# Kernel optimization log

Hardware: AMD Instinct MI355X
Metric: run time of the kernel (lower is better)

Reference implementation:

```python
import jax, jax.numpy as jnp
import numpy as np

N = 50000   # nodes
E = 640000  # edges
IN = 256    # in_dim
H = 128     # hidden
OUT = 40    # out_dim
EPS = 1e-5  # BatchNorm eps


def setup_inputs() -> dict:
    key = jax.random.key(0)
    ks = jax.random.split(key, 14)
    x = jax.random.normal(ks[0], (N, IN), jnp.float32)
    edge_index = jax.random.randint(ks[1], (2, E), 0, N)
    def lin(k, fan_in, shape):
        return jax.random.normal(k, shape, jnp.float32) / np.float32(np.sqrt(fan_in))
    return {
        "x": x,
        "edge_index": edge_index,
        # block 0 (256 -> 128, has res_proj)
        "W0": lin(ks[2], IN, (IN, H)),
        "b0": jnp.zeros((H,), jnp.float32),
        "g0": jnp.ones((H,), jnp.float32),
        "be0": jnp.zeros((H,), jnp.float32),
        "pW": lin(ks[3], IN, (IN, H)),
        "pb": jnp.zeros((H,), jnp.float32),
        # block 1 (128 -> 128, identity residual)
        "W1": lin(ks[4], H, (H, H)),
        "b1": jnp.zeros((H,), jnp.float32),
        "g1": jnp.ones((H,), jnp.float32),
        "be1": jnp.zeros((H,), jnp.float32),
        # head
        "hW": lin(ks[5], H, (H, OUT)),
        "hb": jnp.zeros((OUT,), jnp.float32),
    }


def _gcn_conv(x, W, b, edge_index):
    """GCNConv(improved=True): x' = D^-1/2 (A + 2I) D^-1/2 (x W) + b."""
    h = x @ W  # [N, dout]
    row, col = edge_index[0], edge_index[1]  # source -> target
    # degree of A + 2I (edge_weight = 1, self-loop fill = 2.0)
    deg = jnp.zeros((N,), h.dtype).at[col].add(1.0) + 2.0
    dis = jax.lax.rsqrt(deg)  # deg > 0 always (self-loops)
    norm = dis[row] * dis[col]  # [E]
    # neighbor aggregation: scatter-add normalized messages to targets
    agg = jnp.zeros_like(h).at[col].add(norm[:, None] * h[row])
    # self-loop contribution with weight 2.0
    agg = agg + (2.0 * dis * dis)[:, None] * h
    return agg + b


def _bn(x, gamma, beta):
    # batch statistics (training-mode BatchNorm math), biased variance
    m = jnp.mean(x, axis=0)
    v = jnp.mean(jnp.square(x - m), axis=0)
    return (x - m) * jax.lax.rsqrt(v + EPS) * gamma + beta


def reference(x, edge_index, W0, b0, g0, be0, pW, pb, W1, b1, g1, be1, hW, hb):
    # block 0: conv -> bn -> relu -> (+ res_proj(x))
    out = jax.nn.relu(_bn(_gcn_conv(x, W0, b0, edge_index), g0, be0))
    x1 = out + (x @ pW + pb)
    # block 1: conv -> bn -> relu -> (+ identity)
    out = jax.nn.relu(_bn(_gcn_conv(x1, W1, b1, edge_index), g1, be1))
    x2 = out + x1
    return x2 @ hW + hb  # [N, OUT]
```

## Files before the change

kernel.cpp:

```cpp
#include <hip/hip_runtime.h>

#define H 128
#define IN_DIM 256
#define OUT_DIM 40
#define EPS 1e-5f

typedef unsigned short ushortT;
typedef __attribute__((ext_vector_type(8))) short bf16x8;
typedef __attribute__((ext_vector_type(4))) float f32x4;

static __device__ __forceinline__ ushortT f2bf(float f) {
    union { float f; unsigned u; } v; v.f = f;
    unsigned r = v.u + 0x7FFF + ((v.u >> 16) & 1);
    return (ushortT)(r >> 16);
}
static __device__ __forceinline__ unsigned pk2(float a, float b) {
    return (unsigned)f2bf(a) | ((unsigned)f2bf(b) << 16);
}
static __device__ __forceinline__ float bflo(unsigned v) {
    union { unsigned u; float f; } t; t.u = v << 16; return t.f;
}
static __device__ __forceinline__ float bfhi(unsigned v) {
    union { unsigned u; float f; } t; t.u = v & 0xFFFF0000u; return t.f;
}
static __device__ __forceinline__ float i2f(int v) {
    union { int i; float f; } t; t.i = v; return t.f;
}
static __device__ __forceinline__ int f2i(float v) {
    union { float f; int i; } t; t.f = v; return t.i;
}


__global__ __launch_bounds__(256) void count_xcd(const int* __restrict__ ei, int E, int nper,
                                                 int* __restrict__ cnt) {
    int xcd = blockIdx.x & 7;
    int nchunk = gridDim.x >> 3;
    int chunk = blockIdx.x >> 3;
    int csz = (E + nchunk - 1) / nchunk;
    int beg = chunk * csz;
    int end = min(E, beg + csz);
    for (int e = beg + (int)threadIdx.x; e < end; e += 256) {
        int c = ei[E + e];
        if (c / nper == xcd) atomicAdd(&cnt[c], 1);
    }
}

__global__ __launch_bounds__(256) void scan_block_sum(const int* __restrict__ cnt, int* __restrict__ bsum,
                                                      float* __restrict__ dis, int N) {
    __shared__ int s[256];
    int i = blockIdx.x * 256 + threadIdx.x;
    int c = (i < N) ? cnt[i] : -1;
    int v = (i < N) ? c + 1 : 0;
    if (i < N) dis[i] = rsqrtf((float)c + 2.0f);
    s[threadIdx.x] = v;
    __syncthreads();
    for (int o = 128; o > 0; o >>= 1) {
        if (threadIdx.x < o) s[threadIdx.x] += s[threadIdx.x + o];
        __syncthreads();
    }
    if (threadIdx.x == 0) bsum[blockIdx.x] = s[0];
}

__global__ void scan_tops(const int* __restrict__ bsum, int* __restrict__ boff, int* __restrict__ rowptrN, int nb) {
    __shared__ int s[256];
    int t = threadIdx.x;
    int v = (t < nb) ? bsum[t] : 0;
    s[t] = v;
    __syncthreads();
    for (int o = 1; o < 256; o <<= 1) {
        int u = (t >= o) ? s[t - o] : 0;
        __syncthreads();
        s[t] += u;
        __syncthreads();
    }
    if (t < nb) boff[t] = s[t] - v;
    if (t == 255) *rowptrN = s[255];
}

__global__ __launch_bounds__(256) void scan_final(const int* __restrict__ cnt, const int* __restrict__ boff,
                                                  const float* __restrict__ dis,
                                                  int* __restrict__ rowptr, int* __restrict__ cursor,
                                                  int2* __restrict__ recs, int N) {
    __shared__ int s[256];
    int t = threadIdx.x;
    int i = blockIdx.x * 256 + t;
    int v = (i < N) ? cnt[i] + 1 : 0;
    s[t] = v;
    __syncthreads();
    for (int o = 1; o < 256; o <<= 1) {
        int u = (t >= o) ? s[t - o] : 0;
        __syncthreads();
        s[t] += u;
        __syncthreads();
    }
    if (i < N) {
        int e = boff[blockIdx.x] + s[t] - v;
        rowptr[i] = e;
        cursor[i] = e + 1;
        float d = dis[i];
        int2 r; r.x = i; r.y = f2i(2.0f * d * d);
        recs[e] = r;
    }
}

__global__ __launch_bounds__(256) void fill_xcd(const int* __restrict__ ei, int E, int nper,
                                                const float* __restrict__ dis,
                                                int* __restrict__ cursor, int2* __restrict__ recs) {
    int xcd = blockIdx.x & 7;
    int nchunk = gridDim.x >> 3;
    int chunk = blockIdx.x >> 3;
    int csz = (E + nchunk - 1) / nchunk;
    int beg = chunk * csz;
    int end = min(E, beg + csz);
    for (int e = beg + (int)threadIdx.x; e < end; e += 256) {
        int c = ei[E + e];
        if (c / nper == xcd) {
            int r = ei[e];
            int slot = atomicAdd(&cursor[c], 1);
            int2 rec; rec.x = r; rec.y = f2i(dis[r] * dis[c]);
            recs[slot] = rec;
        }
    }
}


__global__ __launch_bounds__(256) void prep_weights(const float* __restrict__ W0, const float* __restrict__ pW,
                                                    const float* __restrict__ W1, const float* __restrict__ hW,
                                                    ushortT* __restrict__ Wt0, ushortT* __restrict__ WtP,
                                                    ushortT* __restrict__ Wt1, ushortT* __restrict__ WtH,
                                                    int* __restrict__ cnt, float* __restrict__ stats, int N) {
    int i = blockIdx.x * 256 + threadIdx.x;
    if (i < 32768) { int n = i >> 8, k = i & 255; Wt0[i] = f2bf(W0[k * 128 + n]); WtP[i] = f2bf(pW[k * 128 + n]); }
    if (i < 16384) { int n = i >> 7, k = i & 127; Wt1[i] = f2bf(W1[k * 128 + n]); }
    if (i < 6144)  { int n = i >> 7, k = i & 127; WtH[i] = (n < OUT_DIM) ? f2bf(hW[k * OUT_DIM + n]) : (ushortT)0; }
    if (i < N) cnt[i] = 0;
    if (i < 512) stats[i] = 0.f;
}


static __device__ __forceinline__ void g0_loads(const float* __restrict__ X, int brow, int kc,
                                                int tid, int N, float4 pf[4]) {
#pragma unroll
    for (int i = 0; i < 4; ++i) {
        int idx = i * 512 + tid;
        int row = idx >> 5, c4 = idx & 31;
        int gr = brow + row;
        pf[i] = make_float4(0.f, 0.f, 0.f, 0.f);
        if (gr < N) pf[i] = *(const float4*)&X[(size_t)gr * IN_DIM + kc * 128 + c4 * 4];
    }
}
static __device__ __forceinline__ void g0_write(ushortT* __restrict__ Sbuf, int tid, const float4 pf[4]) {
#pragma unroll
    for (int i = 0; i < 4; ++i) {
        int idx = i * 512 + tid;
        int row = idx >> 5, c4 = idx & 31;
        uint2 p;
        p.x = pk2(pf[i].x, pf[i].y);
        p.y = pk2(pf[i].z, pf[i].w);
        *(uint2*)&Sbuf[row * 136 + c4 * 4] = p;
    }
}

__global__ __launch_bounds__(512) void mgemm0d(const float* __restrict__ X,
                                               const ushortT* __restrict__ Wt0,
                                               const ushortT* __restrict__ WtP,
                                               const float* __restrict__ pb,
                                               ushortT* __restrict__ Oh,
                                               ushortT* __restrict__ Op,
                                               int N) {
    __shared__ __align__(16) ushortT S2[2][64 * 136];
    int tid = threadIdx.x;
    int brow = blockIdx.x * 64;
    int w = tid >> 6, lane = tid & 63;
    int lm = lane & 15, lk = lane >> 4;
    int mat = w >> 2;
    int colbase = (w & 3) * 32;
    const ushortT* Wt = mat ? WtP : Wt0;

    bf16x8 breg[2][8];
#pragma unroll
    for (int nt = 0; nt < 2; ++nt)
#pragma unroll
        for (int kk = 0; kk < 8; ++kk)
            breg[nt][kk] = *(const bf16x8*)&Wt[(size_t)(colbase + nt * 16 + lm) * IN_DIM + kk * 32 + lk * 8];
    float bb[2];
    bb[0] = mat ? pb[colbase + lm] : 0.f;
    bb[1] = mat ? pb[colbase + 16 + lm] : 0.f;

    float4 pf[4];
    g0_loads(X, brow, 0, tid, N, pf);
    g0_write(S2[0], tid, pf);
    __syncthreads();
    g0_loads(X, brow, 1, tid, N, pf);

    f32x4 acc[4][2];
#pragma unroll
    for (int mt = 0; mt < 4; ++mt)
#pragma unroll
        for (int nt = 0; nt < 2; ++nt) acc[mt][nt] = (f32x4)0.f;

#pragma unroll
    for (int kk = 0; kk < 4; ++kk) {
        bf16x8 af[4];
#pragma unroll
        for (int mt = 0; mt < 4; ++mt)
            af[mt] = *(const bf16x8*)&S2[0][(mt * 16 + lm) * 136 + kk * 32 + lk * 8];
#pragma unroll
        for (int nt = 0; nt < 2; ++nt)
#pragma unroll
            for (int mt = 0; mt < 4; ++mt)
                acc[mt][nt] = __builtin_amdgcn_mfma_f32_16x16x32_bf16(af[mt], breg[nt][kk], acc[mt][nt], 0, 0, 0);
    }
    g0_write(S2[1], tid, pf);
    __syncthreads();
#pragma unroll
    for (int kk = 0; kk < 4; ++kk) {
        bf16x8 af[4];
#pragma unroll
        for (int mt = 0; mt < 4; ++mt)
            af[mt] = *(const bf16x8*)&S2[1][(mt * 16 + lm) * 136 + kk * 32 + lk * 8];
#pragma unroll
        for (int nt = 0; nt < 2; ++nt)
#pragma unroll
            for (int mt = 0; mt < 4; ++mt)
                acc[mt][nt] = __builtin_amdgcn_mfma_f32_16x16x32_bf16(af[mt], breg[nt][4 + kk], acc[mt][nt], 0, 0, 0);
    }
    __syncthreads();
#pragma unroll
    for (int mt = 0; mt < 4; ++mt)
#pragma unroll
        for (int nt = 0; nt < 2; ++nt) {
            int col = colbase + nt * 16 + lm;
#pragma unroll
            for (int j = 0; j < 4; ++j) {
                int row = mt * 16 + lk * 4 + j;
                S2[mat][row * 136 + col] = f2bf(acc[mt][nt][j] + bb[nt]);
            }
        }
    __syncthreads();
#pragma unroll
    for (int i = 0; i < 4; ++i) {
        int idx = i * 512 + tid;
        int m2 = idx >> 10;
        int rem = idx & 1023;
        int row = rem >> 4, colq = rem & 15;
        int gr = brow + row;
        if (gr < N) {
            uint4 v = *(const uint4*)&S2[m2][row * 136 + colq * 8];
            ushortT* O = m2 ? Op : Oh;
            *(uint4*)&O[(size_t)gr * 128 + colq * 8] = v;
        }
    }
}


__global__ __launch_bounds__(512) void mgemm1_fused(const uint4* __restrict__ aggb,
                                                    const uint4* __restrict__ projb,
                                                    const float* __restrict__ stats,
                                                    const float* __restrict__ g,
                                                    const float* __restrict__ be,
                                                    const ushortT* __restrict__ Wt1,
                                                    ushortT* __restrict__ O,
                                                    uint4* __restrict__ x1b,
                                                    int N) {
    __shared__ __align__(16) ushortT S[17408];
    __shared__ float sc[128], sh[128];
    int tid = threadIdx.x;
    int brow = blockIdx.x * 128;

    if (tid < 128) {
        float mean = stats[tid] / (float)N;
        float var = stats[128 + tid] / (float)N - mean * mean;
        float inv = rsqrtf(var + EPS);
        float s = g[tid] * inv;
        sc[tid] = s;
        sh[tid] = be[tid] - mean * s;
    }
    __syncthreads();

#pragma unroll
    for (int i = 0; i < 4; ++i) {
        int idx = i * 512 + tid;
        int row = idx >> 4, q = idx & 15;
        int gr = brow + row;
        uint4 a = make_uint4(0u, 0u, 0u, 0u), p = a;
        if (gr < N) {
            size_t gidx = (size_t)gr * 16 + q;
            a = aggb[gidx];
            p = projb[gidx];
        }
        int ch = q * 8;
        float v0 = fmaxf(fmaf(bflo(a.x), sc[ch + 0], sh[ch + 0]), 0.f) + bflo(p.x);
        float v1 = fmaxf(fmaf(bfhi(a.x), sc[ch + 1], sh[ch + 1]), 0.f) + bfhi(p.x);
        float v2 = fmaxf(fmaf(bflo(a.y), sc[ch + 2], sh[ch + 2]), 0.f) + bflo(p.y);
        float v3 = fmaxf(fmaf(bfhi(a.y), sc[ch + 3], sh[ch + 3]), 0.f) + bfhi(p.y);
        float v4 = fmaxf(fmaf(bflo(a.z), sc[ch + 4], sh[ch + 4]), 0.f) + bflo(p.z);
        float v5 = fmaxf(fmaf(bfhi(a.z), sc[ch + 5], sh[ch + 5]), 0.f) + bfhi(p.z);
        float v6 = fmaxf(fmaf(bflo(a.w), sc[ch + 6], sh[ch + 6]), 0.f) + bflo(p.w);
        float v7 = fmaxf(fmaf(bfhi(a.w), sc[ch + 7], sh[ch + 7]), 0.f) + bfhi(p.w);
        uint4 pv;
        pv.x = pk2(v0, v1);
        pv.y = pk2(v2, v3);
        pv.z = pk2(v4, v5);
        pv.w = pk2(v6, v7);
        *(uint4*)&S[row * 136 + q * 8] = pv;
        if (gr < N) x1b[(size_t)gr * 16 + q] = pv;
    }
    __syncthreads();

    int w = tid >> 6, lane = tid & 63;
    int lm = lane & 15, lk = lane >> 4;
    int rh = (w >> 2) * 64;
    int colbase = (w & 3) * 32;

    bf16x8 breg[2][4];
#pragma unroll
    for (int nt = 0; nt < 2; ++nt)
#pragma unroll
        for (int ks = 0; ks < 4; ++ks)
            breg[nt][ks] = *(const bf16x8*)&Wt1[(size_t)(colbase + nt * 16 + lm) * H + ks * 32 + lk * 8];

    f32x4 acc[4][2];
#pragma unroll
    for (int mt = 0; mt < 4; ++mt)
#pragma unroll
        for (int nt = 0; nt < 2; ++nt) acc[mt][nt] = (f32x4)0.f;

#pragma unroll
    for (int ks = 0; ks < 4; ++ks) {
        bf16x8 af[4];
#pragma unroll
        for (int mt = 0; mt < 4; ++mt)
            af[mt] = *(const bf16x8*)&S[(rh + mt * 16 + lm) * 136 + ks * 32 + lk * 8];
#pragma unroll
        for (int nt = 0; nt < 2; ++nt)
#pragma unroll
            for (int mt = 0; mt < 4; ++mt)
                acc[mt][nt] = __builtin_amdgcn_mfma_f32_16x16x32_bf16(af[mt], breg[nt][ks], acc[mt][nt], 0, 0, 0);
    }

    __syncthreads();
#pragma unroll
    for (int mt = 0; mt < 4; ++mt)
#pragma unroll
        for (int nt = 0; nt < 2; ++nt) {
            int col = colbase + nt * 16 + lm;
#pragma unroll
            for (int j = 0; j < 4; ++j) {
                int row = rh + mt * 16 + lk * 4 + j;
                S[row * 136 + col] = f2bf(acc[mt][nt][j]);
            }
        }
    __syncthreads();
#pragma unroll
    for (int i = 0; i < 4; ++i) {
        int idx = i * 512 + tid;
        int row = idx >> 4, colq = idx & 15;
        int gr = brow + row;
        if (gr < N) {
            uint4 v = *(const uint4*)&S[row * 136 + colq * 8];
            *(uint4*)&O[(size_t)gr * 128 + colq * 8] = v;
        }
    }
}


__global__ __launch_bounds__(256) void aggregate_rec(const ushortT* __restrict__ h,
                                                     const int* __restrict__ rowptr,
                                                     const int2* __restrict__ recs,
                                                     ushortT* __restrict__ aggb, int N) {
    int n = blockIdx.x * 4 + (threadIdx.x >> 6);
    if (n >= N) return;
    int lane = threadIdx.x & 63;
    int half = lane >> 5, cl = lane & 31;
    int beg = rowptr[n], end = rowptr[n + 1];
    const uint2* h2 = (const uint2*)h;
    float a0 = 0.f, a1 = 0.f, a2 = 0.f, a3 = 0.f;
    float b0 = 0.f, b1 = 0.f, b2 = 0.f, b3 = 0.f;
    int idx = beg + half;
    for (; idx + 2 < end; idx += 4) {
        int2 r0 = recs[idx];
        int2 r1 = recs[idx + 2];
        uint2 v0 = h2[(size_t)r0.x * 32 + cl];
        uint2 v1 = h2[(size_t)r1.x * 32 + cl];
        float n0 = i2f(r0.y), n1 = i2f(r1.y);
        a0 = fmaf(n0, bflo(v0.x), a0); a1 = fmaf(n0, bfhi(v0.x), a1);
        a2 = fmaf(n0, bflo(v0.y), a2); a3 = fmaf(n0, bfhi(v0.y), a3);
        b0 = fmaf(n1, bflo(v1.x), b0); b1 = fmaf(n1, bfhi(v1.x), b1);
        b2 = fmaf(n1, bflo(v1.y), b2); b3 = fmaf(n1, bfhi(v1.y), b3);
    }
    if (idx < end) {
        int2 r0 = recs[idx];
        uint2 v0 = h2[(size_t)r0.x * 32 + cl];
        float n0 = i2f(r0.y);
        a0 = fmaf(n0, bflo(v0.x), a0); a1 = fmaf(n0, bfhi(v0.x), a1);
        a2 = fmaf(n0, bflo(v0.y), a2); a3 = fmaf(n0, bfhi(v0.y), a3);
    }
    a0 += b0; a1 += b1; a2 += b2; a3 += b3;
    a0 += __shfl_xor(a0, 32);
    a1 += __shfl_xor(a1, 32);
    a2 += __shfl_xor(a2, 32);
    a3 += __shfl_xor(a3, 32);
    if (half == 0) {
        uint2 o;
        o.x = pk2(a0, a1);
        o.y = pk2(a2, a3);
        ((uint2*)aggb)[(size_t)n * 32 + cl] = o;
    }
}


__global__ __launch_bounds__(256) void stats_bf(const unsigned* __restrict__ v, int totalU,
                                                float* __restrict__ sums) {
    int tid = blockIdx.x * 256 + threadIdx.x;
    int stride = gridDim.x * 256;
    float sx = 0.f, sy = 0.f, qx = 0.f, qy = 0.f;
    for (int i = tid; i < totalU; i += stride) {
        unsigned u = v[i];
        float a = bflo(u), b = bfhi(u);
        sx += a; sy += b;
        qx = fmaf(a, a, qx); qy = fmaf(b, b, qy);
    }
    __shared__ float l0[256], l1[256], l2[256], l3[256];
    int t = threadIdx.x;
    l0[t] = sx; l1[t] = sy; l2[t] = qx; l3[t] = qy;
    __syncthreads();
    if (t < 64) {
        sx = (l0[t] + l0[t + 64]) + (l0[t + 128] + l0[t + 192]);
        sy = (l1[t] + l1[t + 64]) + (l1[t + 128] + l1[t + 192]);
        qx = (l2[t] + l2[t + 64]) + (l2[t + 128] + l2[t + 192]);
        qy = (l3[t] + l3[t + 64]) + (l3[t + 128] + l3[t + 192]);
        atomicAdd(&sums[2 * t], sx);
        atomicAdd(&sums[2 * t + 1], sy);
        atomicAdd(&sums[128 + 2 * t], qx);
        atomicAdd(&sums[128 + 2 * t + 1], qy);
    }
}


__global__ __launch_bounds__(256) void head_fused(const uint4* __restrict__ aggb,
                                                  const uint4* __restrict__ x1b,
                                                  const float* __restrict__ stats,
                                                  const float* __restrict__ g,
                                                  const float* __restrict__ be,
                                                  const ushortT* __restrict__ WtH,
                                                  const float* __restrict__ hb,
                                                  float* __restrict__ out, int N) {
    __shared__ __align__(16) ushortT As[64][136];
    __shared__ __align__(16) ushortT Bs[48][136];
    __shared__ float sc[128], sh[128];

    int tid = threadIdx.x;
    int brow = blockIdx.x * 64;
    int w = tid >> 6, lane = tid & 63;
    int lm = lane & 15, lk = lane >> 4;

    if (tid < 128) {
        float mean = stats[tid] / (float)N;
        float var = stats[128 + tid] / (float)N - mean * mean;
        float inv = rsqrtf(var + EPS);
        float s = g[tid] * inv;
        sc[tid] = s;
        sh[tid] = be[tid] - mean * s;
    }
    if (tid < 192) {
        int row = tid >> 2, q = tid & 3;
        const uint4* src = (const uint4*)&WtH[(size_t)row * H + q * 32];
        uint4 a = src[0], b = src[1], c = src[2], d = src[3];
        uint4* dst = (uint4*)&Bs[row][q * 32];
        dst[0] = a; dst[1] = b; dst[2] = c; dst[3] = d;
    }
    __syncthreads();
#pragma unroll
    for (int k = 0; k < 4; ++k) {
        int idx = k * 256 + tid;
        int row = idx >> 4, colq = idx & 15;
        int gr = brow + row;
        uint4 a = make_uint4(0u, 0u, 0u, 0u), x = a;
        if (gr < N) {
            size_t gidx = (size_t)brow * 16 + idx;
            a = aggb[gidx];
            x = x1b[gidx];
        }
        int ch = colq * 8;
        float v0 = fmaxf(fmaf(bflo(a.x), sc[ch + 0], sh[ch + 0]), 0.f) + bflo(x.x);
        float v1 = fmaxf(fmaf(bfhi(a.x), sc[ch + 1], sh[ch + 1]), 0.f) + bfhi(x.x);
        float v2 = fmaxf(fmaf(bflo(a.y), sc[ch + 2], sh[ch + 2]), 0.f) + bflo(x.y);
        float v3 = fmaxf(fmaf(bfhi(a.y), sc[ch + 3], sh[ch + 3]), 0.f) + bfhi(x.y);
        float v4 = fmaxf(fmaf(bflo(a.z), sc[ch + 4], sh[ch + 4]), 0.f) + bflo(x.z);
        float v5 = fmaxf(fmaf(bfhi(a.z), sc[ch + 5], sh[ch + 5]), 0.f) + bfhi(x.z);
        float v6 = fmaxf(fmaf(bflo(a.w), sc[ch + 6], sh[ch + 6]), 0.f) + bflo(x.w);
        float v7 = fmaxf(fmaf(bfhi(a.w), sc[ch + 7], sh[ch + 7]), 0.f) + bfhi(x.w);
        uint4 pv;
        pv.x = pk2(v0, v1);
        pv.y = pk2(v2, v3);
        pv.z = pk2(v4, v5);
        pv.w = pk2(v6, v7);
        *(uint4*)&As[row][colq * 8] = pv;
    }
    __syncthreads();

    f32x4 acc[3];
#pragma unroll
    for (int nt = 0; nt < 3; ++nt) acc[nt] = (f32x4)0.f;
#pragma unroll
    for (int ks = 0; ks < 4; ++ks) {
        bf16x8 a = *(const bf16x8*)&As[w * 16 + lm][ks * 32 + lk * 8];
#pragma unroll
        for (int nt = 0; nt < 3; ++nt) {
            bf16x8 b = *(const bf16x8*)&Bs[nt * 16 + lm][ks * 32 + lk * 8];
            acc[nt] = __builtin_amdgcn_mfma_f32_16x16x32_bf16(a, b, acc[nt], 0, 0, 0);
        }
    }
#pragma unroll
    for (int nt = 0; nt < 3; ++nt) {
        int col = nt * 16 + lm;
        if (col < OUT_DIM) {
            float bbv = hb[col];
#pragma unroll
            for (int j = 0; j < 4; ++j) {
                int r = brow + w * 16 + lk * 4 + j;
                if (r < N) out[(size_t)r * OUT_DIM + col] = acc[nt][j] + bbv;
            }
        }
    }
}


extern "C" void kernel_launch(void* const* d_in, const int* in_sizes, int n_in,
                              void* d_out, int out_size, void* d_ws, size_t ws_size,
                              hipStream_t stream) {
    const float* x   = (const float*)d_in[0];
    const int*   ei  = (const int*)d_in[1];
    const float* W0  = (const float*)d_in[2];
    const float* g0  = (const float*)d_in[4];
    const float* be0 = (const float*)d_in[5];
    const float* pW  = (const float*)d_in[6];
    const float* pb  = (const float*)d_in[7];
    const float* W1  = (const float*)d_in[8];
    const float* g1  = (const float*)d_in[10];
    const float* be1 = (const float*)d_in[11];
    const float* hW  = (const float*)d_in[12];
    const float* hb  = (const float*)d_in[13];
    float* out = (float*)d_out;

    int N = in_sizes[0] / IN_DIM;
    int E = in_sizes[1] / 2;
    size_t NH = (size_t)N * H;

    ushortT* hb16   = (ushortT*)d_ws;
    ushortT* aggb   = hb16 + NH;
    ushortT* projb  = aggb + NH;
    ushortT* x1b    = projb + NH;
    float*   dis    = (float*)(x1b + NH);
    int*     cnt    = (int*)(dis + N);
    int*     rowptr = cnt + N;
    int*     cursor = rowptr + (N + 1);
    int2*    recs   = (int2*)(cursor + N);
    float*   stats  = (float*)(recs + (E + N));
    ushortT* Wt0    = (ushortT*)(stats + 512);
    ushortT* WtP    = Wt0 + 128 * 256;
    ushortT* Wt1    = WtP + 128 * 256;
    ushortT* WtH    = Wt1 + 128 * 128;
    int*     bsum   = (int*)(WtH + 48 * 128);
    int*     boff   = bsum + 256;
    float*   stats0 = stats;
    float*   stats1 = stats + 256;

    int nb = (N + 255) / 256;
    int g64 = (N + 63) / 64;
    int g128 = (N + 127) / 128;
    int gAgg = (N + 3) / 4;

    prep_weights<<<196, 256, 0, stream>>>(W0, pW, W1, hW, Wt0, WtP, Wt1, WtH, cnt, stats, N);
    count_xcd<<<2048, 256, 0, stream>>>(ei, E, (N + 7) / 8, cnt);
    scan_block_sum<<<nb, 256, 0, stream>>>(cnt, bsum, dis, N);
    scan_tops<<<1, 256, 0, stream>>>(bsum, boff, &rowptr[N], nb);
    scan_final<<<nb, 256, 0, stream>>>(cnt, boff, dis, rowptr, cursor, recs, N);
    fill_xcd<<<2048, 256, 0, stream>>>(ei, E, (N + 7) / 8, dis, cursor, recs);

    mgemm0d<<<g64, 512, 0, stream>>>(x, Wt0, WtP, pb, hb16, projb, N);
    aggregate_rec<<<gAgg, 256, 0, stream>>>(hb16, rowptr, recs, aggb, N);
    stats_bf<<<256, 256, 0, stream>>>((const unsigned*)aggb, (int)(NH / 2), stats0);

    mgemm1_fused<<<g128, 512, 0, stream>>>((const uint4*)aggb, (const uint4*)projb, stats0, g0, be0,
                                           Wt1, hb16, (uint4*)x1b, N);
    aggregate_rec<<<gAgg, 256, 0, stream>>>(hb16, rowptr, recs, aggb, N);
    stats_bf<<<256, 256, 0, stream>>>((const unsigned*)aggb, (int)(NH / 2), stats1);

    head_fused<<<g64, 256, 0, stream>>>((const uint4*)aggb, (const uint4*)x1b, stats1, g1, be1,
                                        WtH, hb, out, N);
}
```

Before: 251.7 us.

## Fuse degree counting into gemm0 launch and BN stats into aggregation

The edge-degree counting kernel is merged into the first GEMM launch as extra blocks, so the independent count work runs concurrently with the x@W0/x@pW GEMM. The separate stats_bf pass is removed: a persistent-grid aggregation kernel accumulates per-feature sums and sums of squares on the rounded bf16 outputs, using shared-memory then global atomics. This drops two launches and one full reread of the aggregated tensor per layer. In exchange the aggregation loses one-node-per-wave launch granularity, adds atomic contention, and halves the count blocks' thread efficiency.

```diff
diff --git a/kernel.cpp b/kernel.cpp
--- a/kernel.cpp
+++ b/kernel.cpp
@@ -31,19 +31,153 @@
 }
 
 
-__global__ __launch_bounds__(256) void count_xcd(const int* __restrict__ ei, int E, int nper,
-                                                 int* __restrict__ cnt) {
-    int xcd = blockIdx.x & 7;
-    int nchunk = gridDim.x >> 3;
-    int chunk = blockIdx.x >> 3;
-    int csz = (E + nchunk - 1) / nchunk;
-    int beg = chunk * csz;
-    int end = min(E, beg + csz);
-    for (int e = beg + (int)threadIdx.x; e < end; e += 256) {
-        int c = ei[E + e];
-        if (c / nper == xcd) atomicAdd(&cnt[c], 1);
-    }
-}
+__global__ __launch_bounds__(256) void prep_weights(const float* __restrict__ W0, const float* __restrict__ pW,
+                                                    const float* __restrict__ W1, const float* __restrict__ hW,
+                                                    ushortT* __restrict__ Wt0, ushortT* __restrict__ WtP,
+                                                    ushortT* __restrict__ Wt1, ushortT* __restrict__ WtH,
+                                                    int* __restrict__ cnt, float* __restrict__ stats, int N) {
+    int i = blockIdx.x * 256 + threadIdx.x;
+    if (i < 32768) { int n = i >> 8, k = i & 255; Wt0[i] = f2bf(W0[k * 128 + n]); WtP[i] = f2bf(pW[k * 128 + n]); }
+    if (i < 16384) { int n = i >> 7, k = i & 127; Wt1[i] = f2bf(W1[k * 128 + n]); }
+    if (i < 6144)  { int n = i >> 7, k = i & 127; WtH[i] = (n < OUT_DIM) ? f2bf(hW[k * OUT_DIM + n]) : (ushortT)0; }
+    if (i < N) cnt[i] = 0;
+    if (i < 512) stats[i] = 0.f;
+}
+
+
+static __device__ __forceinline__ void g0_loads(const float* __restrict__ X, int brow, int kc,
+                                                int tid, int N, float4 pf[4]) {
+#pragma unroll
+    for (int i = 0; i < 4; ++i) {
+        int idx = i * 512 + tid;
+        int row = idx >> 5, c4 = idx & 31;
+        int gr = brow + row;
+        pf[i] = make_float4(0.f, 0.f, 0.f, 0.f);
+        if (gr < N) pf[i] = *(const float4*)&X[(size_t)gr * IN_DIM + kc * 128 + c4 * 4];
+    }
+}
+static __device__ __forceinline__ void g0_write(ushortT* __restrict__ Sbuf, int tid, const float4 pf[4]) {
+#pragma unroll
+    for (int i = 0; i < 4; ++i) {
+        int idx = i * 512 + tid;
+        int row = idx >> 5, c4 = idx & 31;
+        uint2 p;
+        p.x = pk2(pf[i].x, pf[i].y);
+        p.y = pk2(pf[i].z, pf[i].w);
+        *(uint2*)&Sbuf[row * 136 + c4 * 4] = p;
+    }
+}
+
+__global__ __launch_bounds__(512) void gemm0_count(const float* __restrict__ X,
+                                                   const ushortT* __restrict__ Wt0,
+                                                   const ushortT* __restrict__ WtP,
+                                                   const float* __restrict__ pb,
+                                                   ushortT* __restrict__ Oh,
+                                                   ushortT* __restrict__ Op,
+                                                   const int* __restrict__ ei,
+                                                   int* __restrict__ cnt,
+                                                   int N, int E, int nper, int gemmBlocks) {
+    __shared__ __align__(16) ushortT S2[2][64 * 136];
+    int tid = threadIdx.x;
+
+    if (blockIdx.x >= gemmBlocks) {
+        int cbid = blockIdx.x - gemmBlocks;
+        int xcd = cbid & 7;
+        int nchunk = (gridDim.x - gemmBlocks) >> 3;
+        int chunk = cbid >> 3;
+        int csz = (E + nchunk - 1) / nchunk;
+        int beg = chunk * csz;
+        int end = min(E, beg + csz);
+        for (int e = beg + tid; e < end; e += 512) {
+            int c = ei[E + e];
+            if (c / nper == xcd) atomicAdd(&cnt[c], 1);
+        }
+        return;
+    }
+
+    int brow = blockIdx.x * 64;
+    int w = tid >> 6, lane = tid & 63;
+    int lm = lane & 15, lk = lane >> 4;
+    int mat = w >> 2;
+    int colbase = (w & 3) * 32;
+    const ushortT* Wt = mat ? WtP : Wt0;
+
+    bf16x8 breg[2][8];
+#pragma unroll
+    for (int nt = 0; nt < 2; ++nt)
+#pragma unroll
+        for (int kk = 0; kk < 8; ++kk)
+            breg[nt][kk] = *(const bf16x8*)&Wt[(size_t)(colbase + nt * 16 + lm) * IN_DIM + kk * 32 + lk * 8];
+    float bb[2];
+    bb[0] = mat ? pb[colbase + lm] : 0.f;
+    bb[1] = mat ? pb[colbase + 16 + lm] : 0.f;
+
+    float4 pf[4];
+    g0_loads(X, brow, 0, tid, N, pf);
+    g0_write(S2[0], tid, pf);
+    __syncthreads();
+    g0_loads(X, brow, 1, tid, N, pf);
+
+    f32x4 acc[4][2];
+#pragma unroll
+    for (int mt = 0; mt < 4; ++mt)
+#pragma unroll
+        for (int nt = 0; nt < 2; ++nt) acc[mt][nt] = (f32x4)0.f;
+
+#pragma unroll
+    for (int kk = 0; kk < 4; ++kk) {
+        bf16x8 af[4];
+#pragma unroll
+        for (int mt = 0; mt < 4; ++mt)
+            af[mt] = *(const bf16x8*)&S2[0][(mt * 16 + lm) * 136 + kk * 32 + lk * 8];
+#pragma unroll
+        for (int nt = 0; nt < 2; ++nt)
+#pragma unroll
+            for (int mt = 0; mt < 4; ++mt)
+                acc[mt][nt] = __builtin_amdgcn_mfma_f32_16x16x32_bf16(af[mt], breg[nt][kk], acc[mt][nt], 0, 0, 0);
+    }
+    g0_write(S2[1], tid, pf);
+    __syncthreads();
+#pragma unroll
+    for (int kk = 0; kk < 4; ++kk) {
+        bf16x8 af[4];
+#pragma unroll
+        for (int mt = 0; mt < 4; ++mt)
+            af[mt] = *(const bf16x8*)&S2[1][(mt * 16 + lm) * 136 + kk * 32 + lk * 8];
+#pragma unroll
+        for (int nt = 0; nt < 2; ++nt)
+#pragma unroll
+            for (int mt = 0; mt < 4; ++mt)
+                acc[mt][nt] = __builtin_amdgcn_mfma_f32_16x16x32_bf16(af[mt], breg[nt][4 + kk], acc[mt][nt], 0, 0, 0);
+    }
+    __syncthreads();
+#pragma unroll
+    for (int mt = 0; mt < 4; ++mt)
+#pragma unroll
+        for (int nt = 0; nt < 2; ++nt) {
+            int col = colbase + nt * 16 + lm;
+#pragma unroll
+            for (int j = 0; j < 4; ++j) {
+                int row = mt * 16 + lk * 4 + j;
+                S2[mat][row * 136 + col] = f2bf(acc[mt][nt][j] + bb[nt]);
+            }
+        }
+    __syncthreads();
+#pragma unroll
+    for (int i = 0; i < 4; ++i) {
+        int idx = i * 512 + tid;
+        int m2 = idx >> 10;
+        int rem = idx & 1023;
+        int row = rem >> 4, colq = rem & 15;
+        int gr = brow + row;
+        if (gr < N) {
+            uint4 v = *(const uint4*)&S2[m2][row * 136 + colq * 8];
+            ushortT* O = m2 ? Op : Oh;
+            *(uint4*)&O[(size_t)gr * 128 + colq * 8] = v;
+        }
+    }
+}
+
 
 __global__ __launch_bounds__(256) void scan_block_sum(const int* __restrict__ cnt, int* __restrict__ bsum,
                                                       float* __restrict__ dis, int N) {
@@ -124,133 +258,73 @@
 }
 
 
-__global__ __launch_bounds__(256) void prep_weights(const float* __restrict__ W0, const float* __restrict__ pW,
-                                                    const float* __restrict__ W1, const float* __restrict__ hW,
-                                                    ushortT* __restrict__ Wt0, ushortT* __restrict__ WtP,
-                                                    ushortT* __restrict__ Wt1, ushortT* __restrict__ WtH,
-                                                    int* __restrict__ cnt, float* __restrict__ stats, int N) {
-    int i = blockIdx.x * 256 + threadIdx.x;
-    if (i < 32768) { int n = i >> 8, k = i & 255; Wt0[i] = f2bf(W0[k * 128 + n]); WtP[i] = f2bf(pW[k * 128 + n]); }
-    if (i < 16384) { int n = i >> 7, k = i & 127; Wt1[i] = f2bf(W1[k * 128 + n]); }
-    if (i < 6144)  { int n = i >> 7, k = i & 127; WtH[i] = (n < OUT_DIM) ? f2bf(hW[k * OUT_DIM + n]) : (ushortT)0; }
-    if (i < N) cnt[i] = 0;
-    if (i < 512) stats[i] = 0.f;
-}
-
-
-static __device__ __forceinline__ void g0_loads(const float* __restrict__ X, int brow, int kc,
-                                                int tid, int N, float4 pf[4]) {
-#pragma unroll
-    for (int i = 0; i < 4; ++i) {
-        int idx = i * 512 + tid;
-        int row = idx >> 5, c4 = idx & 31;
-        int gr = brow + row;
-        pf[i] = make_float4(0.f, 0.f, 0.f, 0.f);
-        if (gr < N) pf[i] = *(const float4*)&X[(size_t)gr * IN_DIM + kc * 128 + c4 * 4];
-    }
-}
-static __device__ __forceinline__ void g0_write(ushortT* __restrict__ Sbuf, int tid, const float4 pf[4]) {
-#pragma unroll
-    for (int i = 0; i < 4; ++i) {
-        int idx = i * 512 + tid;
-        int row = idx >> 5, c4 = idx & 31;
-        uint2 p;
-        p.x = pk2(pf[i].x, pf[i].y);
-        p.y = pk2(pf[i].z, pf[i].w);
-        *(uint2*)&Sbuf[row * 136 + c4 * 4] = p;
-    }
-}
-
-__global__ __launch_bounds__(512) void mgemm0d(const float* __restrict__ X,
-                                               const ushortT* __restrict__ Wt0,
-                                               const ushortT* __restrict__ WtP,
-                                               const float* __restrict__ pb,
-                                               ushortT* __restrict__ Oh,
-                                               ushortT* __restrict__ Op,
-                                               int N) {
-    __shared__ __align__(16) ushortT S2[2][64 * 136];
+__global__ __launch_bounds__(256) void aggregate_stats(const ushortT* __restrict__ h,
+                                                       const int* __restrict__ rowptr,
+                                                       const int2* __restrict__ recs,
+                                                       ushortT* __restrict__ aggb,
+                                                       float* __restrict__ stats, int N) {
+    __shared__ float sumL[128], sqL[128];
     int tid = threadIdx.x;
-    int brow = blockIdx.x * 64;
-    int w = tid >> 6, lane = tid & 63;
-    int lm = lane & 15, lk = lane >> 4;
-    int mat = w >> 2;
-    int colbase = (w & 3) * 32;
-    const ushortT* Wt = mat ? WtP : Wt0;
-
-    bf16x8 breg[2][8];
-#pragma unroll
-    for (int nt = 0; nt < 2; ++nt)
-#pragma unroll
-        for (int kk = 0; kk < 8; ++kk)
-            breg[nt][kk] = *(const bf16x8*)&Wt[(size_t)(colbase + nt * 16 + lm) * IN_DIM + kk * 32 + lk * 8];
-    float bb[2];
-    bb[0] = mat ? pb[colbase + lm] : 0.f;
-    bb[1] = mat ? pb[colbase + 16 + lm] : 0.f;
-
-    float4 pf[4];
-    g0_loads(X, brow, 0, tid, N, pf);
-    g0_write(S2[0], tid, pf);
-    __syncthreads();
-    g0_loads(X, brow, 1, tid, N, pf);
-
-    f32x4 acc[4][2];
-#pragma unroll
-    for (int mt = 0; mt < 4; ++mt)
-#pragma unroll
-        for (int nt = 0; nt < 2; ++nt) acc[mt][nt] = (f32x4)0.f;
-
-#pragma unroll
-    for (int kk = 0; kk < 4; ++kk) {
-        bf16x8 af[4];
-#pragma unroll
-        for (int mt = 0; mt < 4; ++mt)
-            af[mt] = *(const bf16x8*)&S2[0][(mt * 16 + lm) * 136 + kk * 32 + lk * 8];
-#pragma unroll
-        for (int nt = 0; nt < 2; ++nt)
-#pragma unroll
-            for (int mt = 0; mt < 4; ++mt)
-                acc[mt][nt] = __builtin_amdgcn_mfma_f32_16x16x32_bf16(af[mt], breg[nt][kk], acc[mt][nt], 0, 0, 0);
-    }
-    g0_write(S2[1], tid, pf);
-    __syncthreads();
-#pragma unroll
-    for (int kk = 0; kk < 4; ++kk) {
-        bf16x8 af[4];
-#pragma unroll
-        for (int mt = 0; mt < 4; ++mt)
-            af[mt] = *(const bf16x8*)&S2[1][(mt * 16 + lm) * 136 + kk * 32 + lk * 8];
-#pragma unroll
-        for (int nt = 0; nt < 2; ++nt)
-#pragma unroll
-            for (int mt = 0; mt < 4; ++mt)
-                acc[mt][nt] = __builtin_amdgcn_mfma_f32_16x16x32_bf16(af[mt], breg[nt][4 + kk], acc[mt][nt], 0, 0, 0);
-    }
-    __syncthreads();
-#pragma unroll
-    for (int mt = 0; mt < 4; ++mt)
-#pragma unroll
-        for (int nt = 0; nt < 2; ++nt) {
-            int col = colbase + nt * 16 + lm;
-#pragma unroll
-            for (int j = 0; j < 4; ++j) {
-                int row = mt * 16 + lk * 4 + j;
-                S2[mat][row * 136 + col] = f2bf(acc[mt][nt][j] + bb[nt]);
-            }
-        }
-    __syncthreads();
-#pragma unroll
-    for (int i = 0; i < 4; ++i) {
-        int idx = i * 512 + tid;
-        int m2 = idx >> 10;
-        int rem = idx & 1023;
-        int row = rem >> 4, colq = rem & 15;
-        int gr = brow + row;
-        if (gr < N) {
-            uint4 v = *(const uint4*)&S2[m2][row * 136 + colq * 8];
-            ushortT* O = m2 ? Op : Oh;
-            *(uint4*)&O[(size_t)gr * 128 + colq * 8] = v;
-        }
-    }
+    if (tid < 128) { sumL[tid] = 0.f; sqL[tid] = 0.f; }
+    __syncthreads();
+
+    int wv = tid >> 6, lane = tid & 63;
+    int half = lane >> 5, cl = lane & 31;
+    const uint2* h2 = (const uint2*)h;
+    float s0 = 0.f, s1 = 0.f, s2 = 0.f, s3 = 0.f;
+
+    int stride = gridDim.x * 4;
+    for (int n = blockIdx.x * 4 + wv; n < N; n += stride) {
+        int beg = rowptr[n], end = rowptr[n + 1];
+        float a0 = 0.f, a1 = 0.f, a2 = 0.f, a3 = 0.f;
+        float b0 = 0.f, b1 = 0.f, b2 = 0.f, b3 = 0.f;
+        int idx = beg + half;
+        for (; idx + 2 < end; idx += 4) {
+            int2 r0 = recs[idx];
+            int2 r1 = recs[idx + 2];
+            uint2 v0 = h2[(size_t)r0.x * 32 + cl];
+            uint2 v1 = h2[(size_t)r1.x * 32 + cl];
+            float n0 = i2f(r0.y), n1 = i2f(r1.y);
+            a0 = fmaf(n0, bflo(v0.x), a0); a1 = fmaf(n0, bfhi(v0.x), a1);
+            a2 = fmaf(n0, bflo(v0.y), a2); a3 = fmaf(n0, bfhi(v0.y), a3);
+            b0 = fmaf(n1, bflo(v1.x), b0); b1 = fmaf(n1, bfhi(v1.x), b1);
+            b2 = fmaf(n1, bflo(v1.y), b2); b3 = fmaf(n1, bfhi(v1.y), b3);
+        }
+        if (idx < end) {
+            int2 r0 = recs[idx];
+            uint2 v0 = h2[(size_t)r0.x * 32 + cl];
+            float n0 = i2f(r0.y);
+            a0 = fmaf(n0, bflo(v0.x), a0); a1 = fmaf(n0, bfhi(v0.x), a1);
+            a2 = fmaf(n0, bflo(v0.y), a2); a3 = fmaf(n0, bfhi(v0.y), a3);
+        }
+        a0 += b0; a1 += b1; a2 += b2; a3 += b3;
+        a0 += __shfl_xor(a0, 32);
+        a1 += __shfl_xor(a1, 32);
+        a2 += __shfl_xor(a2, 32);
+        a3 += __shfl_xor(a3, 32);
+        unsigned ox = pk2(a0, a1);
+        unsigned oy = pk2(a2, a3);
+        if (half == 0) {
+            uint2 o; o.x = ox; o.y = oy;
+            ((uint2*)aggb)[(size_t)n * 32 + cl] = o;
+        }
+        float r0 = bflo(ox), r1 = bfhi(ox), r2 = bflo(oy), r3 = bfhi(oy);
+        if (half == 0) {
+            s0 += r0; s1 += r1; s2 += r2; s3 += r3;
+        } else {
+            s0 = fmaf(r0, r0, s0); s1 = fmaf(r1, r1, s1);
+            s2 = fmaf(r2, r2, s2); s3 = fmaf(r3, r3, s3);
+        }
+    }
+
+    float* dst = half ? sqL : sumL;
+    atomicAdd(&dst[4 * cl + 0], s0);
+    atomicAdd(&dst[4 * cl + 1], s1);
+    atomicAdd(&dst[4 * cl + 2], s2);
+    atomicAdd(&dst[4 * cl + 3], s3);
+    __syncthreads();
+    if (tid < 128) atomicAdd(&stats[tid], sumL[tid]);
+    else atomicAdd(&stats[tid], sqL[tid - 128]);
 }
 
 
@@ -361,79 +435,6 @@
             uint4 v = *(const uint4*)&S[row * 136 + colq * 8];
             *(uint4*)&O[(size_t)gr * 128 + colq * 8] = v;
         }
-    }
-}
-
-
-__global__ __launch_bounds__(256) void aggregate_rec(const ushortT* __restrict__ h,
-                                                     const int* __restrict__ rowptr,
-                                                     const int2* __restrict__ recs,
-                                                     ushortT* __restrict__ aggb, int N) {
-    int n = blockIdx.x * 4 + (threadIdx.x >> 6);
-    if (n >= N) return;
-    int lane = threadIdx.x & 63;
-    int half = lane >> 5, cl = lane & 31;
-    int beg = rowptr[n], end = rowptr[n + 1];
-    const uint2* h2 = (const uint2*)h;
-    float a0 = 0.f, a1 = 0.f, a2 = 0.f, a3 = 0.f;
-    float b0 = 0.f, b1 = 0.f, b2 = 0.f, b3 = 0.f;
-    int idx = beg + half;
-    for (; idx + 2 < end; idx += 4) {
-        int2 r0 = recs[idx];
-        int2 r1 = recs[idx + 2];
-        uint2 v0 = h2[(size_t)r0.x * 32 + cl];
-        uint2 v1 = h2[(size_t)r1.x * 32 + cl];
-        float n0 = i2f(r0.y), n1 = i2f(r1.y);
-        a0 = fmaf(n0, bflo(v0.x), a0); a1 = fmaf(n0, bfhi(v0.x), a1);
-        a2 = fmaf(n0, bflo(v0.y), a2); a3 = fmaf(n0, bfhi(v0.y), a3);
-        b0 = fmaf(n1, bflo(v1.x), b0); b1 = fmaf(n1, bfhi(v1.x), b1);
-        b2 = fmaf(n1, bflo(v1.y), b2); b3 = fmaf(n1, bfhi(v1.y), b3);
-    }
-    if (idx < end) {
-        int2 r0 = recs[idx];
-        uint2 v0 = h2[(size_t)r0.x * 32 + cl];
-        float n0 = i2f(r0.y);
-        a0 = fmaf(n0, bflo(v0.x), a0); a1 = fmaf(n0, bfhi(v0.x), a1);
-        a2 = fmaf(n0, bflo(v0.y), a2); a3 = fmaf(n0, bfhi(v0.y), a3);
-    }
-    a0 += b0; a1 += b1; a2 += b2; a3 += b3;
-    a0 += __shfl_xor(a0, 32);
-    a1 += __shfl_xor(a1, 32);
-    a2 += __shfl_xor(a2, 32);
-    a3 += __shfl_xor(a3, 32);
-    if (half == 0) {
-        uint2 o;
-        o.x = pk2(a0, a1);
-        o.y = pk2(a2, a3);
-        ((uint2*)aggb)[(size_t)n * 32 + cl] = o;
-    }
-}
-
-
-__global__ __launch_bounds__(256) void stats_bf(const unsigned* __restrict__ v, int totalU,
-                                                float* __restrict__ sums) {
-    int tid = blockIdx.x * 256 + threadIdx.x;
-    int stride = gridDim.x * 256;
-    float sx = 0.f, sy = 0.f, qx = 0.f, qy = 0.f;
-    for (int i = tid; i < totalU; i += stride) {
-        unsigned u = v[i];
-        float a = bflo(u), b = bfhi(u);
-        sx += a; sy += b;
-        qx = fmaf(a, a, qx); qy = fmaf(b, b, qy);
-    }
-    __shared__ float l0[256], l1[256], l2[256], l3[256];
-    int t = threadIdx.x;
-    l0[t] = sx; l1[t] = sy; l2[t] = qx; l3[t] = qy;
-    __syncthreads();
-    if (t < 64) {
-        sx = (l0[t] + l0[t + 64]) + (l0[t + 128] + l0[t + 192]);
-        sy = (l1[t] + l1[t + 64]) + (l1[t + 128] + l1[t + 192]);
-        qx = (l2[t] + l2[t + 64]) + (l2[t + 128] + l2[t + 192]);
-        qy = (l3[t] + l3[t + 64]) + (l3[t + 128] + l3[t + 192]);
-        atomicAdd(&sums[2 * t], sx);
-        atomicAdd(&sums[2 * t + 1], sy);
-        atomicAdd(&sums[128 + 2 * t], qx);
-        atomicAdd(&sums[128 + 2 * t + 1], qy);
     }
 }
 
@@ -570,23 +571,24 @@
     int nb = (N + 255) / 256;
     int g64 = (N + 63) / 64;
     int g128 = (N + 127) / 128;
-    int gAgg = (N + 3) / 4;
+    int nper = (N + 7) / 8;
+    const int CNT_BLOCKS = 1024;
 
     prep_weights<<<196, 256, 0, stream>>>(W0, pW, W1, hW, Wt0, WtP, Wt1, WtH, cnt, stats, N);
-    count_xcd<<<2048, 256, 0, stream>>>(ei, E, (N + 7) / 8, cnt);
+
+    gemm0_count<<<g64 + CNT_BLOCKS, 512, 0, stream>>>(x, Wt0, WtP, pb, hb16, projb,
+                                                      ei, cnt, N, E, nper, g64);
+
     scan_block_sum<<<nb, 256, 0, stream>>>(cnt, bsum, dis, N);
     scan_tops<<<1, 256, 0, stream>>>(bsum, boff, &rowptr[N], nb);
     scan_final<<<nb, 256, 0, stream>>>(cnt, boff, dis, rowptr, cursor, recs, N);
-    fill_xcd<<<2048, 256, 0, stream>>>(ei, E, (N + 7) / 8, dis, cursor, recs);
-
-    mgemm0d<<<g64, 512, 0, stream>>>(x, Wt0, WtP, pb, hb16, projb, N);
-    aggregate_rec<<<gAgg, 256, 0, stream>>>(hb16, rowptr, recs, aggb, N);
-    stats_bf<<<256, 256, 0, stream>>>((const unsigned*)aggb, (int)(NH / 2), stats0);
+    fill_xcd<<<2048, 256, 0, stream>>>(ei, E, nper, dis, cursor, recs);
+
+    aggregate_stats<<<2048, 256, 0, stream>>>(hb16, rowptr, recs, aggb, stats0, N);
 
     mgemm1_fused<<<g128, 512, 0, stream>>>((const uint4*)aggb, (const uint4*)projb, stats0, g0, be0,
                                            Wt1, hb16, (uint4*)x1b, N);
-    aggregate_rec<<<gAgg, 256, 0, stream>>>(hb16, rowptr, recs, aggb, N);
-    stats_bf<<<256, 256, 0, stream>>>((const unsigned*)aggb, (int)(NH / 2), stats1);
+    aggregate_stats<<<2048, 256, 0, stream>>>(hb16, rowptr, recs, aggb, stats1, N);
 
     head_fused<<<g64, 256, 0, stream>>>((const uint4*)aggb, (const uint4*)x1b, stats1, g1, be1,
                                         WtH, hb, out, N);
```

After: 316.2 us. 1.26x slower.
